# Kernel tuning notes

Measured on AMD Instinct MI355X. Metric: run time of the kernel, lower is better.

## Reference

```python
import jax, jax.numpy as jnp
import numpy as np

GAMMA = 1.0e6  # sigmoid sharpness for soft histogram


def _dct_basis():
    # Standard orthonormal 8x8 2D DCT-II basis, laid out as [64, 1, 8, 8] (OIHW).
    i = np.arange(8)
    a = np.where(i == 0, np.sqrt(1.0 / 8.0), np.sqrt(2.0 / 8.0))
    cos = np.cos((2 * i[None, :] + 1) * i[:, None] * np.pi / 16.0)  # [freq, pos]
    basis = np.einsum('u,v,ui,vj->uvij', a, a, cos, cos).reshape(64, 1, 8, 8)
    return jnp.asarray(basis, jnp.float32)


def _conv(x, w, stride=1, pad=0):
    return jax.lax.conv_general_dilated(
        x, w, (stride, stride), [(pad, pad), (pad, pad)],
        dimension_numbers=('NCHW', 'OIHW', 'NCHW'))


def _bn(x, g, b, eps=1e-5):
    # BatchNorm2d in training mode: batch statistics over (N, H, W).
    m = x.mean((0, 2, 3), keepdims=True)
    v = x.var((0, 2, 3), keepdims=True)
    return g[None, :, None, None] * (x - m) * jax.lax.rsqrt(v + eps) + b[None, :, None, None]


def _pool2(x):
    return jax.lax.reduce_window(x, -jnp.inf, jax.lax.max,
                                 (1, 1, 2, 2), (1, 1, 2, 2), 'VALID')


def setup_inputs() -> dict:
    key = jax.random.key(0)
    ks = jax.random.split(key, 16)
    B = 64

    def n(k, shape, scale=0.05):
        return jax.random.normal(k, shape, jnp.float32) * scale

    FC1_IN = 15 * 8 * 256 + 64  # 30784
    return {
        'x': jax.random.normal(ks[0], (B, 1, 256, 256), jnp.float32),
        'qvectors': jax.random.uniform(ks[1], (B, 64), dtype=jnp.float32),
        'dct_basis': _dct_basis(),
        'w1a': n(ks[2], (64, 1, 5, 5)), 'b1a': jnp.zeros(64, jnp.float32),
        'g1a': jnp.ones(64, jnp.float32), 'be1a': jnp.zeros(64, jnp.float32),
        'w1b': n(ks[3], (64, 64, 5, 5)), 'b1b': jnp.zeros(64, jnp.float32),
        'g1b': jnp.ones(64, jnp.float32), 'be1b': jnp.zeros(64, jnp.float32),
        'w2a': n(ks[4], (128, 64, 5, 5)), 'b2a': jnp.zeros(128, jnp.float32),
        'g2a': jnp.ones(128, jnp.float32), 'be2a': jnp.zeros(128, jnp.float32),
        'w3a': n(ks[5], (256, 128, 5, 5)), 'b3a': jnp.zeros(256, jnp.float32),
        'g3a': jnp.ones(256, jnp.float32), 'be3a': jnp.zeros(256, jnp.float32),
        'fc1_w': n(ks[6], (500, FC1_IN), 0.02), 'fc1_b': jnp.zeros(500, jnp.float32),
        'fc2_w': n(ks[7], (500, 564), 0.02), 'fc2_b': jnp.zeros(500, jnp.float32),
        'fc3_w': n(ks[8], (2, 564), 0.02), 'fc3_b': jnp.zeros(2, jnp.float32),
    }


def reference(x, qvectors, dct_basis,
              w1a, b1a, g1a, be1a,
              w1b, b1b, g1b, be1b,
              w2a, b2a, g2a, be2a,
              w3a, b3a, g3a, be3a,
              fc1_w, fc1_b, fc2_w, fc2_b, fc3_w, fc3_b):
    # --- no_grad block: DCT + 121-bin soft histogram ---
    xd = _conv(x, dct_basis, stride=8)  # [B, 64, 32, 32]
    bins = jnp.arange(-60, 61, dtype=xd.dtype)  # 121 thresholds

    def step(_, b):
        h = jnp.sum(jax.nn.sigmoid(GAMMA * (xd - b)), axis=(2, 3)) / 1024.0  # [B, 64]
        return None, h

    _, hist = jax.lax.scan(step, None, bins)        # [121, B, 64]
    hist = jnp.transpose(hist, (1, 0, 2))           # [B, 121, 64]
    feat = hist[:, 0:120, :] - hist[:, 1:121, :]    # per-bin soft counts
    feat = jax.lax.stop_gradient(feat.reshape(-1, 1, 120, 64))

    # --- CNN stack ---
    h = jax.nn.relu(_bn(_conv(feat, w1a, pad=2) + b1a[None, :, None, None], g1a, be1a))
    h = jax.nn.relu(_bn(_conv(h, w1b, pad=2) + b1b[None, :, None, None], g1b, be1b))
    h = _pool2(h)  # [B, 64, 60, 32]
    h = jax.nn.relu(_bn(_conv(h, w2a, pad=2) + b2a[None, :, None, None], g2a, be2a))
    h = _pool2(h)  # [B, 128, 30, 16]
    h = jax.nn.relu(_bn(_conv(h, w3a, pad=2) + b3a[None, :, None, None], g3a, be3a))
    h = _pool2(h)  # [B, 256, 15, 8]

    # --- MLP head with qvector concats ---
    hf = h.reshape(-1, 15 * 8 * 256)
    z = jax.nn.relu(jnp.concatenate([qvectors, hf], axis=1) @ fc1_w.T + fc1_b)
    z = jax.nn.relu(jnp.concatenate([qvectors, z], axis=1) @ fc2_w.T + fc2_b)
    return jnp.concatenate([qvectors, z], axis=1) @ fc3_w.T + fc3_b  # [B, 2]
```

## Files before the change

### kernel.cpp

```cpp
#include <hip/hip_runtime.h>
#include <math.h>


typedef __attribute__((ext_vector_type(8))) _Float16 f16x8;
typedef __attribute__((ext_vector_type(4))) float f32x4;

#define GAMMA_F 1.0e6f

__device__ __forceinline__ unsigned short f2h(float f) {
  _Float16 h = (_Float16)f;
  union { _Float16 h; unsigned short u; } x; x.h = h; return x.u;
}
__device__ __forceinline__ float h2f(unsigned short u) {
  union { unsigned short u; _Float16 h; } x; x.u = u; return (float)x.h;
}

__global__ __launch_bounds__(256) void k_dct(const float* __restrict__ x,
                                             const float* __restrict__ basis,
                                             float* __restrict__ xd) {
  __shared__ float bT[4096];
  __shared__ float pix[4][64];
  int tid = threadIdx.x;
  for (int e = tid; e < 4096; e += 256)
    bT[e] = basis[(e & 63) * 64 + (e >> 6)];
  __syncthreads();
  int w = tid >> 6, lane = tid & 63;
  int b = blockIdx.x >> 3;
  int br = ((blockIdx.x & 7) << 2) + w;
  const float* xb = x + (size_t)b * 65536;
  float* xdb = xd + (size_t)b * 65536;
  for (int bc = 0; bc < 32; ++bc) {
    __syncthreads();
    pix[w][lane] = xb[(br * 8 + (lane >> 3)) * 256 + bc * 8 + (lane & 7)];
    __syncthreads();
    float acc = 0.f;
#pragma unroll
    for (int p = 0; p < 64; ++p)
      acc = fmaf(bT[p * 64 + lane], pix[w][p], acc);
    xdb[lane * 1024 + br * 32 + bc] = acc;
  }
}

__global__ __launch_bounds__(256) void k_hist(const float* __restrict__ xd,
                                              float* __restrict__ feat) {
  __shared__ float h[120];
  int tid = threadIdx.x;
  int bc = blockIdx.x;
  int b = bc >> 6, c = bc & 63;
  if (tid < 120) h[tid] = 0.f;
  __syncthreads();
  const float4* p4 = (const float4*)(xd + (size_t)bc * 1024);
  float4 v4 = p4[tid];
#pragma unroll
  for (int k = 0; k < 4; ++k) {
    float pv = k == 0 ? v4.x : (k == 1 ? v4.y : (k == 2 ? v4.z : v4.w));
    float v = rintf(pv);
    float d = pv - v;
    if (fabsf(d) < 2e-5f && v >= -60.f && v <= 60.f) {
      float s = 1.f / (1.f + expf(-GAMMA_F * d));
      int vi = (int)v;
      if (vi >= -59) atomicAdd(&h[vi + 59], 1.f - s);
      if (vi <= 59)  atomicAdd(&h[vi + 60], s);
    } else {
      int j = (int)ceilf(pv + 60.f) - 1;
      if (j >= 0 && j <= 119) atomicAdd(&h[j], 1.f);
    }
  }
  __syncthreads();
  if (tid < 120)
    feat[((size_t)b * 120 + tid) * 64 + c] = h[tid] * (1.f / 1024.f);
}

__global__ __launch_bounds__(256) void k_prepw(const float* __restrict__ w,
                                               unsigned short* __restrict__ wt,
                                               int OC, int IC) {
  int n = OC * IC * 25;
  int idx = blockIdx.x * 256 + threadIdx.x;
  if (idx >= n) return;
  int j = idx & 7;
  int q = (idx >> 3) & 3;
  int l15 = (idx >> 5) & 15;
  int r = idx >> 9;
  int icb = r % (IC / 32);
  int r2 = r / (IC / 32);
  int mt = r2 % (OC / 16);
  int t = r2 / (OC / 16);
  int oc = mt * 16 + l15;
  int ic = icb * 32 + q * 8 + j;
  wt[idx] = f2h(w[((size_t)oc * IC + ic) * 25 + t]);
}

__global__ __launch_bounds__(256) void k_conv1a(const float* __restrict__ in,
                                                const float* __restrict__ wgt,
                                                unsigned short* __restrict__ out) {
  __shared__ float tile[20 * 21];
  int tx = threadIdx.x & 15, ty = threadIdx.x >> 4;
  int tileX = (blockIdx.x & 3) * 16, tileY = (blockIdx.x >> 2) * 16;
  int b = blockIdx.y, ocb = blockIdx.z * 8;
  const float* inc = in + (size_t)b * 7680;
  for (int e = threadIdx.x; e < 400; e += 256) {
    int ly = e / 20, lx = e % 20;
    int gy = tileY - 2 + ly, gx = tileX - 2 + lx;
    float v = 0.f;
    if ((unsigned)gy < 120u && (unsigned)gx < 64u) v = inc[gy * 64 + gx];
    tile[ly * 21 + lx] = v;
  }
  __syncthreads();
  float tv[25];
#pragma unroll
  for (int dy = 0; dy < 5; ++dy)
#pragma unroll
    for (int dx = 0; dx < 5; ++dx)
      tv[dy * 5 + dx] = tile[(ty + dy) * 21 + tx + dx];
  float acc[8];
#pragma unroll
  for (int o = 0; o < 8; ++o) {
    const float* wo = wgt + (size_t)(ocb + o) * 25;
    float a = 0.f;
#pragma unroll
    for (int t = 0; t < 25; ++t) a = fmaf(tv[t], wo[t], a);
    acc[o] = a;
  }
  int oy = tileY + ty, ox = tileX + tx;
  if (oy < 120) {
    size_t base = (((size_t)b * 120 + oy) * 64 + ox) * 64 + ocb;
    ushort4 p0, p1;
    p0.x = f2h(acc[0]); p0.y = f2h(acc[1]); p0.z = f2h(acc[2]); p0.w = f2h(acc[3]);
    p1.x = f2h(acc[4]); p1.y = f2h(acc[5]); p1.z = f2h(acc[6]); p1.w = f2h(acc[7]);
    *(ushort4*)(out + base) = p0;
    *(ushort4*)(out + base + 4) = p1;
  }
}

template <int CIN, int H, int W, int TC, int NT, int OC, bool PREBN>
__global__ __launch_bounds__(256, 3) void k_convM(const unsigned short* __restrict__ in,
                                                  const unsigned short* __restrict__ wt,
                                                  unsigned short* __restrict__ out,
                                                  const float* __restrict__ pst,
                                                  const float* __restrict__ pg,
                                                  const float* __restrict__ pbe) {
  constexpr int XC = TC / 16, RPW = NT / XC, WGR = 4 * RPW;
  constexpr int LW = TC + 4, LR = WGR + 4, NPX = LR * LW;
  constexpr int NXC = W / TC;
  constexpr int MTS = (CIN / 32) * 512;
  constexpr int TS = (OC / 16) * MTS;
  __shared__ unsigned short lds[NPX * 40];
  int tid = threadIdx.x;
  int w = tid >> 6, lane = tid & 63, l15 = lane & 15, q = lane >> 4;
  int q4 = tid & 3;
  int ry = blockIdx.x / NXC, cx = blockIdx.x % NXC;
  int y0 = ry * WGR, x0 = cx * TC;
  int b = blockIdx.y, oc0 = blockIdx.z * 64;
  int z4 = blockIdx.z * 4;
  int lofs = (l15 * 4 + q) * 8;
  f32x4 acc[4][NT];
#pragma unroll
  for (int mt = 0; mt < 4; ++mt)
#pragma unroll
    for (int nt = 0; nt < NT; ++nt) acc[mt][nt] = 0.f;

  for (int icb = 0; icb < CIN / 32; ++icb) {
    float s8[8], a8[8];
    if (PREBN) {
      int cb = icb * 32 + q4 * 8;
#pragma unroll
      for (int j = 0; j < 8; ++j) {
        float m = pst[cb + j], iv = pst[CIN + cb + j];
        s8[j] = pg[cb + j] * iv;
        a8[j] = pbe[cb + j] - m * s8[j];
      }
    }
    __syncthreads();
    for (int e = tid; e < NPX * 4; e += 256) {
      int px = e >> 2;
      int lr = px / LW, c = px % LW;
      int y = y0 - 2 + lr, x = x0 - 2 + c;
      f16x8 v = (f16x8)0;
      if ((unsigned)y < (unsigned)H && (unsigned)x < (unsigned)W) {
        v = *(const f16x8*)(in + (((size_t)b * H + y) * W + x) * CIN + icb * 32 + q4 * 8);
        if (PREBN) {
#pragma unroll
          for (int j = 0; j < 8; ++j) {
            float f = fmaf((float)v[j], s8[j], a8[j]);
            v[j] = (_Float16)(f > 0.f ? f : 0.f);
          }
        }
      }
      *(f16x8*)&lds[(size_t)(px * 5 + q4) * 8] = v;
    }
    __syncthreads();
    const unsigned short* wbase = wt + (size_t)icb * 512 + lofs;
    f16x8 avn[4];
#pragma unroll
    for (int mt = 0; mt < 4; ++mt)
      avn[mt] = *(const f16x8*)(wbase + (size_t)(z4 + mt) * MTS);
#pragma unroll
    for (int t = 0; t < 25; ++t) {
      int dy = t / 5, dx = t % 5;
      f16x8 avc[4];
#pragma unroll
      for (int mt = 0; mt < 4; ++mt) avc[mt] = avn[mt];
      if (t < 24) {
#pragma unroll
        for (int mt = 0; mt < 4; ++mt)
          avn[mt] = *(const f16x8*)(wbase + (size_t)(t + 1) * TS + (size_t)(z4 + mt) * MTS);
      }
#pragma unroll
      for (int nt = 0; nt < NT; ++nt) {
        int lr = w * RPW + nt / XC + dy;
        int c = (nt % XC) * 16 + l15 + dx;
        f16x8 bv = *(const f16x8*)&lds[(size_t)((lr * LW + c) * 5 + q) * 8];
#pragma unroll
        for (int mt = 0; mt < 4; ++mt)
          acc[mt][nt] = __builtin_amdgcn_mfma_f32_16x16x32_f16(avc[mt], bv, acc[mt][nt], 0, 0, 0);
      }
    }
  }
#pragma unroll
  for (int nt = 0; nt < NT; ++nt) {
    int y = y0 + w * RPW + nt / XC;
    if (y >= H) continue;
    int x = x0 + (nt % XC) * 16 + l15;
    size_t pbase = (((size_t)b * H + y) * W + x) * OC + oc0 + q * 4;
#pragma unroll
    for (int mt = 0; mt < 4; ++mt) {
      ushort4 pk;
      pk.x = f2h(acc[mt][nt][0]);
      pk.y = f2h(acc[mt][nt][1]);
      pk.z = f2h(acc[mt][nt][2]);
      pk.w = f2h(acc[mt][nt][3]);
      *(ushort4*)(out + pbase + mt * 16) = pk;
    }
  }
}

template <int C>
__global__ __launch_bounds__(256) void k_bnstatsv(const unsigned short* __restrict__ x,
                                                  float* __restrict__ acc,
                                                  int nIter) {
  constexpr int CV = C / 8, KPB = 256 / CV;
  __shared__ float r1[256][8], r2[256][8];
  int tid = threadIdx.x;
  int cv = tid % CV, kq = tid / CV;
  size_t row0 = (size_t)blockIdx.x * (KPB * nIter) + kq;
  const unsigned short* p = x + row0 * C + cv * 8;
  float s1[8], s2[8];
#pragma unroll
  for (int j = 0; j < 8; ++j) { s1[j] = 0.f; s2[j] = 0.f; }
  for (int it = 0; it < nIter; ++it) {
    f16x8 v = *(const f16x8*)(p + (size_t)it * KPB * C);
#pragma unroll
    for (int j = 0; j < 8; ++j) {
      float f = (float)v[j];
      s1[j] += f;
      s2[j] += f * f;
    }
  }
#pragma unroll
  for (int j = 0; j < 8; ++j) { r1[tid][j] = s1[j]; r2[tid][j] = s2[j]; }
  __syncthreads();
  if (tid < C) {
    int cv0 = tid >> 3, e = tid & 7;
    float t1 = 0.f, t2 = 0.f;
    for (int k = 0; k < KPB; ++k) {
      t1 += r1[k * CV + cv0][e];
      t2 += r2[k * CV + cv0][e];
    }
    atomicAdd(&acc[tid], t1);
    atomicAdd(&acc[C + tid], t2);
  }
}

__global__ __launch_bounds__(256) void k_bnfin(const float* __restrict__ acc,
                                               float* __restrict__ stats,
                                               int C, float invN) {
  int c = threadIdx.x + blockIdx.x * 256;
  if (c >= C) return;
  float m = acc[c] * invN;
  float v = acc[C + c] * invN - m * m;
  stats[c] = m;
  stats[C + c] = rsqrtf(v + 1e-5f);
}

template <int C, int H, int W>
__global__ __launch_bounds__(256) void k_brp(const unsigned short* __restrict__ x,
                                             unsigned short* __restrict__ y,
                                             const float* __restrict__ stats,
                                             const float* __restrict__ g,
                                             const float* __restrict__ be) {
  constexpr int OH = H / 2, OW = W / 2, CV = C / 8;
  int idx = blockIdx.x * 256 + threadIdx.x;
  int cv = idx % CV;
  int t = idx / CV;
  int ox = t % OW; t /= OW;
  int oy = t % OH;
  int b = t / OH;
  int c0 = cv * 8;
  const unsigned short* p = x + ((size_t)(b * H + oy * 2) * W + ox * 2) * C + c0;
  f16x8 v00 = *(const f16x8*)p;
  f16x8 v01 = *(const f16x8*)(p + C);
  f16x8 v10 = *(const f16x8*)(p + (size_t)W * C);
  f16x8 v11 = *(const f16x8*)(p + (size_t)W * C + C);
  f16x8 r;
#pragma unroll
  for (int j = 0; j < 8; ++j) {
    int c = c0 + j;
    float m = stats[c], iv = stats[C + c], gg = g[c], bb = be[c];
    float f0 = gg * (((float)v00[j] - m) * iv) + bb;
    float f1 = gg * (((float)v01[j] - m) * iv) + bb;
    float f2 = gg * (((float)v10[j] - m) * iv) + bb;
    float f3 = gg * (((float)v11[j] - m) * iv) + bb;
    f0 = f0 > 0.f ? f0 : 0.f;
    f1 = f1 > 0.f ? f1 : 0.f;
    f2 = f2 > 0.f ? f2 : 0.f;
    f3 = f3 > 0.f ? f3 : 0.f;
    float r01 = f0 > f1 ? f0 : f1;
    float r23 = f2 > f3 ? f2 : f3;
    r[j] = (_Float16)(r01 > r23 ? r01 : r23);
  }
  *(f16x8*)(y + (size_t)idx * 8) = r;
}

__global__ __launch_bounds__(256) void k_brp3t(const unsigned short* __restrict__ x,
                                               unsigned short* __restrict__ actT,
                                               const float* __restrict__ stats,
                                               const float* __restrict__ g,
                                               const float* __restrict__ be) {
  __shared__ float tile[64 * 65];
  int s = blockIdx.x;
  int oy = s >> 3, ox = s & 7;
  int ci = threadIdx.x & 63, bq = threadIdx.x >> 6;
  for (int cs = 0; cs < 4; ++cs) {
    int c = cs * 64 + ci;
    float m = stats[c], iv = stats[256 + c], gg = g[c], bb = be[c];
    __syncthreads();
    for (int b = bq; b < 64; b += 4) {
      float mx = 0.f;
#pragma unroll
      for (int qq = 0; qq < 4; ++qq) {
        int yy = oy * 2 + (qq >> 1), xx = ox * 2 + (qq & 1);
        float v = h2f(x[((size_t)(b * 30 + yy) * 16 + xx) * 256 + c]);
        v = gg * ((v - m) * iv) + bb;
        v = v > 0.f ? v : 0.f;
        mx = v > mx ? v : mx;
      }
      tile[ci * 65 + b] = mx;
    }
    __syncthreads();
    for (int e = threadIdx.x; e < 4096; e += 256) {
      int cc = e >> 6, bb2 = e & 63;
      actT[(size_t)bb2 * 30784 + 64 + (cs * 64 + cc) * 120 + s] = f2h(tile[cc * 65 + bb2]);
    }
  }
}

__global__ __launch_bounds__(256) void k_qinit(const float* __restrict__ q,
                                               unsigned short* __restrict__ actT,
                                               float* __restrict__ in2T,
                                               float* __restrict__ in3T,
                                               float* __restrict__ z1pre,
                                               float* __restrict__ bnacc) {
  int idx = blockIdx.x * 256 + threadIdx.x;
  if (idx < 32000) z1pre[idx] = 0.f;
  else if (idx < 33024) bnacc[idx - 32000] = 0.f;
  if (idx >= 4096) return;
  int b = idx >> 6, i = idx & 63;
  float v = q[idx];
  actT[(size_t)b * 30784 + i] = f2h(v);
  in2T[i * 64 + b] = v;
  in3T[i * 64 + b] = v;
}

__global__ __launch_bounds__(256) void k_fc1m(const unsigned short* __restrict__ actT,
                                              const float* __restrict__ wgt,
                                              float* __restrict__ z1pre) {
  constexpr int IN = 30784;
  constexpr int KSTEPS = IN / 32;
  __shared__ float part[4][16][64];
  int tid = threadIdx.x;
  int w = tid >> 6, lane = tid & 63, l15 = lane & 15, q = lane >> 4;
  int ob = blockIdx.x * 16;
  int row = ob + l15; if (row > 499) row = 499;
  int kw = blockIdx.y * 4 + w;
  f32x4 acc[4];
#pragma unroll
  for (int nt = 0; nt < 4; ++nt) acc[nt] = 0.f;
  for (int s = kw; s < KSTEPS; s += 32) {
    int k0 = s * 32;
    const float4* wp = (const float4*)(wgt + (size_t)row * IN + k0 + q * 8);
    float4 wa = wp[0], wb = wp[1];
    f16x8 a;
    a[0] = (_Float16)wa.x; a[1] = (_Float16)wa.y;
    a[2] = (_Float16)wa.z; a[3] = (_Float16)wa.w;
    a[4] = (_Float16)wb.x; a[5] = (_Float16)wb.y;
    a[6] = (_Float16)wb.z; a[7] = (_Float16)wb.w;
#pragma unroll
    for (int nt = 0; nt < 4; ++nt) {
      f16x8 bv = *(const f16x8*)(actT + (size_t)(nt * 16 + l15) * IN + k0 + q * 8);
      acc[nt] = __builtin_amdgcn_mfma_f32_16x16x32_f16(a, bv, acc[nt], 0, 0, 0);
    }
  }
#pragma unroll
  for (int nt = 0; nt < 4; ++nt)
#pragma unroll
    for (int reg = 0; reg < 4; ++reg)
      part[w][q * 4 + reg][nt * 16 + l15] = acc[nt][reg];
  __syncthreads();
  for (int e = tid; e < 1024; e += 256) {
    int m = e >> 6, n = e & 63;
    float sum = part[0][m][n] + part[1][m][n] + part[2][m][n] + part[3][m][n];
    int o = ob + m;
    if (o < 500) atomicAdd(&z1pre[o * 64 + n], sum);
  }
}

__global__ __launch_bounds__(256) void k_fc1ep(const float* __restrict__ z1pre,
                                               const float* __restrict__ bias,
                                               float* __restrict__ in2T) {
  int idx = blockIdx.x * 256 + threadIdx.x;
  if (idx >= 500 * 64) return;
  int o = idx >> 6;
  float v = z1pre[idx] + bias[o];
  in2T[idx + 64 * 64] = v > 0.f ? v : 0.f;
}

__global__ __launch_bounds__(256) void k_fc_small(const float* __restrict__ inT,
                                                  const float* __restrict__ wgt,
                                                  const float* __restrict__ bias,
                                                  float* __restrict__ out,
                                                  int IN, int mode) {
  __shared__ float part[4][64];
  int o = blockIdx.x;
  int lane = threadIdx.x & 63, w = threadIdx.x >> 6;
  float acc = 0.f;
  for (int i = w; i < IN; i += 4)
    acc = fmaf(inT[(size_t)i * 64 + lane], wgt[(size_t)o * IN + i], acc);
  part[w][lane] = acc;
  __syncthreads();
  if (threadIdx.x < 64) {
    float s = part[0][lane] + part[1][lane] + part[2][lane] + part[3][lane] + bias[o];
    if (mode == 0) {
      s = s > 0.f ? s : 0.f;
      out[(64 + o) * 64 + lane] = s;
    } else {
      out[lane * 2 + o] = s;
    }
  }
}

extern "C" void kernel_launch(void* const* d_in, const int* in_sizes, int n_in,
                              void* d_out, int out_size, void* d_ws, size_t ws_size,
                              hipStream_t stream) {
  const float* x      = (const float*)d_in[0];
  const float* qvec   = (const float*)d_in[1];
  const float* basis  = (const float*)d_in[2];
  const float* w1a    = (const float*)d_in[3];
  const float* g1a    = (const float*)d_in[5];
  const float* be1a   = (const float*)d_in[6];
  const float* w1b    = (const float*)d_in[7];
  const float* g1b    = (const float*)d_in[9];
  const float* be1b   = (const float*)d_in[10];
  const float* w2a    = (const float*)d_in[11];
  const float* g2a    = (const float*)d_in[13];
  const float* be2a   = (const float*)d_in[14];
  const float* w3a    = (const float*)d_in[15];
  const float* g3a    = (const float*)d_in[17];
  const float* be3a   = (const float*)d_in[18];
  const float* fc1w   = (const float*)d_in[19];
  const float* fc1b   = (const float*)d_in[20];
  const float* fc2w   = (const float*)d_in[21];
  const float* fc2b   = (const float*)d_in[22];
  const float* fc3w   = (const float*)d_in[23];
  const float* fc3b   = (const float*)d_in[24];
  float* out = (float*)d_out;

  char* base = (char*)d_ws;
  constexpr size_t ARENA = 62914560;
  char* arenaA = base;
  char* arenaB = base + ARENA;
  char* sm     = base + 2 * ARENA;

  float*          xd   = (float*)arenaA;
  unsigned short* A    = (unsigned short*)arenaA;
  unsigned short* P1   = (unsigned short*)arenaA;
  unsigned short* P2   = (unsigned short*)arenaA;
  unsigned short* actT = (unsigned short*)arenaA;

  float*          feat = (float*)arenaB;
  unsigned short* Bb   = (unsigned short*)arenaB;
  unsigned short* C2   = (unsigned short*)arenaB;
  unsigned short* D3   = (unsigned short*)arenaB;

  float* in2T = (float*)sm;
  float* in3T = (float*)(sm + 144384);
  float* z1p  = (float*)(sm + 288768);
  float* ACC  = (float*)(sm + 416768);
  float* S1A  = (float*)(sm + 420864);
  float* S1B  = (float*)(sm + 421376);
  float* S2A  = (float*)(sm + 421888);
  float* S3A  = (float*)(sm + 422912);
  unsigned short* WT1 = (unsigned short*)(sm + 424960);
  unsigned short* WT2 = (unsigned short*)(sm + 834560);
  unsigned short* WT3 = (unsigned short*)(sm + 1653760);

  k_qinit<<<130, 256, 0, stream>>>(qvec, actT, in2T, in3T, z1p, ACC);
  k_prepw<<<400, 256, 0, stream>>>(w1b, WT1, 64, 64);
  k_prepw<<<800, 256, 0, stream>>>(w2a, WT2, 128, 64);
  k_prepw<<<3200, 256, 0, stream>>>(w3a, WT3, 256, 128);

  k_dct<<<64 * 8, 256, 0, stream>>>(x, basis, xd);
  k_hist<<<4096, 256, 0, stream>>>(xd, feat);

  k_conv1a<<<dim3(32, 64, 8), 256, 0, stream>>>(feat, w1a, A);
  k_bnstatsv<64><<<240, 256, 0, stream>>>(A, ACC, 64);
  k_bnfin<<<1, 64, 0, stream>>>(ACC, S1A, 64, 1.f / 491520.f);

  k_convM<64, 120, 64, 64, 4, 64, true><<<dim3(30, 64, 1), 256, 0, stream>>>(
      A, WT1, Bb, S1A, g1a, be1a);
  k_bnstatsv<64><<<240, 256, 0, stream>>>(Bb, ACC + 128, 64);
  k_bnfin<<<1, 64, 0, stream>>>(ACC + 128, S1B, 64, 1.f / 491520.f);
  k_brp<64, 120, 64><<<3840, 256, 0, stream>>>(Bb, P1, S1B, g1b, be1b);

  k_convM<64, 60, 32, 32, 4, 128, false><<<dim3(8, 64, 2), 256, 0, stream>>>(
      P1, WT2, C2, S1A, g1a, be1a);
  k_bnstatsv<128><<<240, 256, 0, stream>>>(C2, ACC + 256, 32);
  k_bnfin<<<1, 128, 0, stream>>>(ACC + 256, S2A, 128, 1.f / 122880.f);
  k_brp<128, 60, 32><<<1920, 256, 0, stream>>>(C2, P2, S2A, g2a, be2a);

  k_convM<128, 30, 16, 16, 2, 256, false><<<dim3(4, 64, 4), 256, 0, stream>>>(
      P2, WT3, D3, S1A, g1a, be1a);
  k_bnstatsv<256><<<240, 256, 0, stream>>>(D3, ACC + 512, 16);
  k_bnfin<<<1, 256, 0, stream>>>(ACC + 512, S3A, 256, 1.f / 30720.f);
  k_qinit<<<130, 256, 0, stream>>>(qvec, actT, in2T, in3T, z1p, ACC);
  k_brp3t<<<120, 256, 0, stream>>>(D3, actT, S3A, g3a, be3a);

  k_fc1m<<<dim3(32, 8), 256, 0, stream>>>(actT, fc1w, z1p);
  k_fc1ep<<<125, 256, 0, stream>>>(z1p, fc1b, in2T);
  k_fc_small<<<500, 256, 0, stream>>>(in2T, fc2w, fc2b, in3T, 564, 0);
  k_fc_small<<<2, 256, 0, stream>>>(in3T, fc3w, fc3b, out, 564, 1);
}
```

Baseline: 889.3 us.

## Fuse BatchNorm statistics accumulation into conv epilogues, drop separate stats kernels

The conv1a and the MFMA conv kernels now reduce per-channel sum and sum-of-squares in their epilogues, using wave shuffles and shared memory, then atomically add the totals to the BN accumulator. This removes four k_bnstatsv launches that each re-read the full fp16 activation tensors. The cost is extra epilogue work and more atomics per block. Statistics are now taken from the fp32 accumulators instead of the fp16-rounded values, which changes numerics slightly.

New measurement: 941.0 us. 5.8% more time.

```diff
diff --git a/kernel.cpp b/kernel.cpp
--- a/kernel.cpp
+++ b/kernel.cpp
@@ -92,9 +92,12 @@
 
 __global__ __launch_bounds__(256) void k_conv1a(const float* __restrict__ in,
                                                 const float* __restrict__ wgt,
-                                                unsigned short* __restrict__ out) {
+                                                unsigned short* __restrict__ out,
+                                                float* __restrict__ bnacc) {
   __shared__ float tile[20 * 21];
+  __shared__ float reds[2][4][8];
   int tx = threadIdx.x & 15, ty = threadIdx.x >> 4;
+  int lane = threadIdx.x & 63, wv = threadIdx.x >> 6;
   int tileX = (blockIdx.x & 3) * 16, tileY = (blockIdx.x >> 2) * 16;
   int b = blockIdx.y, ocb = blockIdx.z * 8;
   const float* inc = in + (size_t)b * 7680;
@@ -122,7 +125,8 @@
     acc[o] = a;
   }
   int oy = tileY + ty, ox = tileX + tx;
-  if (oy < 120) {
+  bool valid = oy < 120;
+  if (valid) {
     size_t base = (((size_t)b * 120 + oy) * 64 + ox) * 64 + ocb;
     ushort4 p0, p1;
     p0.x = f2h(acc[0]); p0.y = f2h(acc[1]); p0.z = f2h(acc[2]); p0.w = f2h(acc[3]);
@@ -130,6 +134,23 @@
     *(ushort4*)(out + base) = p0;
     *(ushort4*)(out + base + 4) = p1;
   }
+#pragma unroll
+  for (int o = 0; o < 8; ++o) {
+    float v = valid ? acc[o] : 0.f;
+    float v2 = v * v;
+#pragma unroll
+    for (int m = 1; m < 64; m <<= 1) {
+      v += __shfl_xor(v, m);
+      v2 += __shfl_xor(v2, m);
+    }
+    if (lane == 0) { reds[0][wv][o] = v; reds[1][wv][o] = v2; }
+  }
+  __syncthreads();
+  if (threadIdx.x < 16) {
+    int o = threadIdx.x & 7, s = threadIdx.x >> 3;
+    float t = reds[s][0][o] + reds[s][1][o] + reds[s][2][o] + reds[s][3][o];
+    atomicAdd(&bnacc[s * 64 + ocb + o], t);
+  }
 }
 
 template <int CIN, int H, int W, int TC, int NT, int OC, bool PREBN>
@@ -138,7 +159,8 @@
                                                   unsigned short* __restrict__ out,
                                                   const float* __restrict__ pst,
                                                   const float* __restrict__ pg,
-                                                  const float* __restrict__ pbe) {
+                                                  const float* __restrict__ pbe,
+                                                  float* __restrict__ bnacc) {
   constexpr int XC = TC / 16, RPW = NT / XC, WGR = 4 * RPW;
   constexpr int LW = TC + 4, LR = WGR + 4, NPX = LR * LW;
   constexpr int NXC = W / TC;
@@ -216,6 +238,11 @@
       }
     }
   }
+  float s1[4][4], s2[4][4];
+#pragma unroll
+  for (int mt = 0; mt < 4; ++mt)
+#pragma unroll
+    for (int r = 0; r < 4; ++r) { s1[mt][r] = 0.f; s2[mt][r] = 0.f; }
 #pragma unroll
   for (int nt = 0; nt < NT; ++nt) {
     int y = y0 + w * RPW + nt / XC;
@@ -230,44 +257,45 @@
       pk.z = f2h(acc[mt][nt][2]);
       pk.w = f2h(acc[mt][nt][3]);
       *(ushort4*)(out + pbase + mt * 16) = pk;
-    }
-  }
-}
-
-template <int C>
-__global__ __launch_bounds__(256) void k_bnstatsv(const unsigned short* __restrict__ x,
-                                                  float* __restrict__ acc,
-                                                  int nIter) {
-  constexpr int CV = C / 8, KPB = 256 / CV;
-  __shared__ float r1[256][8], r2[256][8];
-  int tid = threadIdx.x;
-  int cv = tid % CV, kq = tid / CV;
-  size_t row0 = (size_t)blockIdx.x * (KPB * nIter) + kq;
-  const unsigned short* p = x + row0 * C + cv * 8;
-  float s1[8], s2[8];
-#pragma unroll
-  for (int j = 0; j < 8; ++j) { s1[j] = 0.f; s2[j] = 0.f; }
-  for (int it = 0; it < nIter; ++it) {
-    f16x8 v = *(const f16x8*)(p + (size_t)it * KPB * C);
-#pragma unroll
-    for (int j = 0; j < 8; ++j) {
-      float f = (float)v[j];
-      s1[j] += f;
-      s2[j] += f * f;
-    }
-  }
-#pragma unroll
-  for (int j = 0; j < 8; ++j) { r1[tid][j] = s1[j]; r2[tid][j] = s2[j]; }
-  __syncthreads();
-  if (tid < C) {
-    int cv0 = tid >> 3, e = tid & 7;
-    float t1 = 0.f, t2 = 0.f;
-    for (int k = 0; k < KPB; ++k) {
-      t1 += r1[k * CV + cv0][e];
-      t2 += r2[k * CV + cv0][e];
-    }
-    atomicAdd(&acc[tid], t1);
-    atomicAdd(&acc[C + tid], t2);
+#pragma unroll
+      for (int r = 0; r < 4; ++r) {
+        float v = acc[mt][nt][r];
+        s1[mt][r] += v;
+        s2[mt][r] += v * v;
+      }
+    }
+  }
+#pragma unroll
+  for (int mt = 0; mt < 4; ++mt)
+#pragma unroll
+    for (int r = 0; r < 4; ++r) {
+#pragma unroll
+      for (int m = 1; m < 16; m <<= 1) {
+        s1[mt][r] += __shfl_xor(s1[mt][r], m);
+        s2[mt][r] += __shfl_xor(s2[mt][r], m);
+      }
+    }
+  __syncthreads();
+  float* red = (float*)lds;
+  if (l15 == 0) {
+#pragma unroll
+    for (int mt = 0; mt < 4; ++mt)
+#pragma unroll
+      for (int r = 0; r < 4; ++r) {
+        int slot = ((w * 4 + q) * 16 + mt * 4 + r) * 2;
+        red[slot] = s1[mt][r];
+        red[slot + 1] = s2[mt][r];
+      }
+  }
+  __syncthreads();
+  if (tid < 128) {
+    int c = tid & 63, s = tid >> 6;
+    int mt = c >> 4, q2 = (c >> 2) & 3, r = c & 3;
+    float t = 0.f;
+#pragma unroll
+    for (int ww = 0; ww < 4; ++ww)
+      t += red[((ww * 4 + q2) * 16 + mt * 4 + r) * 2 + s];
+    atomicAdd(&bnacc[s * OC + oc0 + c], t);
   }
 }
 
@@ -511,25 +539,21 @@
   k_dct<<<64 * 8, 256, 0, stream>>>(x, basis, xd);
   k_hist<<<4096, 256, 0, stream>>>(xd, feat);
 
-  k_conv1a<<<dim3(32, 64, 8), 256, 0, stream>>>(feat, w1a, A);
-  k_bnstatsv<64><<<240, 256, 0, stream>>>(A, ACC, 64);
+  k_conv1a<<<dim3(32, 64, 8), 256, 0, stream>>>(feat, w1a, A, ACC);
   k_bnfin<<<1, 64, 0, stream>>>(ACC, S1A, 64, 1.f / 491520.f);
 
   k_convM<64, 120, 64, 64, 4, 64, true><<<dim3(30, 64, 1), 256, 0, stream>>>(
-      A, WT1, Bb, S1A, g1a, be1a);
-  k_bnstatsv<64><<<240, 256, 0, stream>>>(Bb, ACC + 128, 64);
+      A, WT1, Bb, S1A, g1a, be1a, ACC + 128);
   k_bnfin<<<1, 64, 0, stream>>>(ACC + 128, S1B, 64, 1.f / 491520.f);
   k_brp<64, 120, 64><<<3840, 256, 0, stream>>>(Bb, P1, S1B, g1b, be1b);
 
   k_convM<64, 60, 32, 32, 4, 128, false><<<dim3(8, 64, 2), 256, 0, stream>>>(
-      P1, WT2, C2, S1A, g1a, be1a);
-  k_bnstatsv<128><<<240, 256, 0, stream>>>(C2, ACC + 256, 32);
+      P1, WT2, C2, S1A, g1a, be1a, ACC + 256);
   k_bnfin<<<1, 128, 0, stream>>>(ACC + 256, S2A, 128, 1.f / 122880.f);
   k_brp<128, 60, 32><<<1920, 256, 0, stream>>>(C2, P2, S2A, g2a, be2a);
 
   k_convM<128, 30, 16, 16, 2, 256, false><<<dim3(4, 64, 4), 256, 0, stream>>>(
-      P2, WT3, D3, S1A, g1a, be1a);
-  k_bnstatsv<256><<<240, 256, 0, stream>>>(D3, ACC + 512, 16);
+      P2, WT3, D3, S1A, g1a, be1a, ACC + 512);
   k_bnfin<<<1, 256, 0, stream>>>(ACC + 512, S3A, 256, 1.f / 30720.f);
   k_qinit<<<130, 256, 0, stream>>>(qvec, actT, in2T, in3T, z1p, ACC);
   k_brp3t<<<120, 256, 0, stream>>>(D3, actT, S3A, g3a, be3a);
```

## Fuse DCT and soft histogram into one kernel with shared-memory partial histograms

Applied to the files above, without the earlier changes.

The DCT kernel now bins each coefficient directly into a per-block shared-memory histogram (64 channels x 120 bins) instead of writing the full DCT image to global memory for a separate histogram kernel. Each block then adds its partial histograms into the feature buffer with global atomics, and the init kernel is enlarged to zero that buffer first. This removes a 16 MB write and re-read plus one launch, at the cost of 30 KB extra shared memory per block (lower occupancy), shared-memory atomic contention, and 7680 global atomics per block across 8 blocks per image. Because the partial sums are added in varying order, results are no longer bit-for-bit deterministic.

Result: slower. 1.040 ms (+16.9%).

```diff
diff --git a/kernel.cpp b/kernel.cpp
--- a/kernel.cpp
+++ b/kernel.cpp
@@ -15,20 +15,21 @@
   union { unsigned short u; _Float16 h; } x; x.u = u; return (float)x.h;
 }
 
-__global__ __launch_bounds__(256) void k_dct(const float* __restrict__ x,
-                                             const float* __restrict__ basis,
-                                             float* __restrict__ xd) {
+__global__ __launch_bounds__(256) void k_dcth(const float* __restrict__ x,
+                                              const float* __restrict__ basis,
+                                              float* __restrict__ feat) {
   __shared__ float bT[4096];
   __shared__ float pix[4][64];
+  __shared__ float hist[64 * 120];
   int tid = threadIdx.x;
   for (int e = tid; e < 4096; e += 256)
     bT[e] = basis[(e & 63) * 64 + (e >> 6)];
+  for (int e = tid; e < 7680; e += 256) hist[e] = 0.f;
   __syncthreads();
   int w = tid >> 6, lane = tid & 63;
   int b = blockIdx.x >> 3;
   int br = ((blockIdx.x & 7) << 2) + w;
   const float* xb = x + (size_t)b * 65536;
-  float* xdb = xd + (size_t)b * 65536;
   for (int bc = 0; bc < 32; ++bc) {
     __syncthreads();
     pix[w][lane] = xb[(br * 8 + (lane >> 3)) * 256 + bc * 8 + (lane & 7)];
@@ -37,38 +38,23 @@
 #pragma unroll
     for (int p = 0; p < 64; ++p)
       acc = fmaf(bT[p * 64 + lane], pix[w][p], acc);
-    xdb[lane * 1024 + br * 32 + bc] = acc;
-  }
-}
-
-__global__ __launch_bounds__(256) void k_hist(const float* __restrict__ xd,
-                                              float* __restrict__ feat) {
-  __shared__ float h[120];
-  int tid = threadIdx.x;
-  int bc = blockIdx.x;
-  int b = bc >> 6, c = bc & 63;
-  if (tid < 120) h[tid] = 0.f;
-  __syncthreads();
-  const float4* p4 = (const float4*)(xd + (size_t)bc * 1024);
-  float4 v4 = p4[tid];
-#pragma unroll
-  for (int k = 0; k < 4; ++k) {
-    float pv = k == 0 ? v4.x : (k == 1 ? v4.y : (k == 2 ? v4.z : v4.w));
-    float v = rintf(pv);
-    float d = pv - v;
+    float v = rintf(acc);
+    float d = acc - v;
     if (fabsf(d) < 2e-5f && v >= -60.f && v <= 60.f) {
       float s = 1.f / (1.f + expf(-GAMMA_F * d));
       int vi = (int)v;
-      if (vi >= -59) atomicAdd(&h[vi + 59], 1.f - s);
-      if (vi <= 59)  atomicAdd(&h[vi + 60], s);
+      if (vi >= -59) atomicAdd(&hist[lane * 120 + vi + 59], 1.f - s);
+      if (vi <= 59)  atomicAdd(&hist[lane * 120 + vi + 60], s);
     } else {
-      int j = (int)ceilf(pv + 60.f) - 1;
-      if (j >= 0 && j <= 119) atomicAdd(&h[j], 1.f);
+      int j = (int)ceilf(acc + 60.f) - 1;
+      if (j >= 0 && j <= 119) atomicAdd(&hist[lane * 120 + j], 1.f);
     }
   }
   __syncthreads();
-  if (tid < 120)
-    feat[((size_t)b * 120 + tid) * 64 + c] = h[tid] * (1.f / 1024.f);
+  for (int e = tid; e < 7680; e += 256) {
+    int c = e / 120, j = e % 120;
+    atomicAdd(&feat[((size_t)b * 120 + j) * 64 + c], hist[e] * (1.f / 1024.f));
+  }
 }
 
 __global__ __launch_bounds__(256) void k_prepw(const float* __restrict__ w,
@@ -359,8 +345,10 @@
                                                float* __restrict__ in2T,
                                                float* __restrict__ in3T,
                                                float* __restrict__ z1pre,
-                                               float* __restrict__ bnacc) {
+                                               float* __restrict__ bnacc,
+                                               float* __restrict__ featz) {
   int idx = blockIdx.x * 256 + threadIdx.x;
+  if (featz && idx < 491520) featz[idx] = 0.f;
   if (idx < 32000) z1pre[idx] = 0.f;
   else if (idx < 33024) bnacc[idx - 32000] = 0.f;
   if (idx >= 4096) return;
@@ -480,7 +468,6 @@
   char* arenaB = base + ARENA;
   char* sm     = base + 2 * ARENA;
 
-  float*          xd   = (float*)arenaA;
   unsigned short* A    = (unsigned short*)arenaA;
   unsigned short* P1   = (unsigned short*)arenaA;
   unsigned short* P2   = (unsigned short*)arenaA;
@@ -503,13 +490,12 @@
   unsigned short* WT2 = (unsigned short*)(sm + 834560);
   unsigned short* WT3 = (unsigned short*)(sm + 1653760);
 
-  k_qinit<<<130, 256, 0, stream>>>(qvec, actT, in2T, in3T, z1p, ACC);
+  k_qinit<<<1920, 256, 0, stream>>>(qvec, actT, in2T, in3T, z1p, ACC, feat);
   k_prepw<<<400, 256, 0, stream>>>(w1b, WT1, 64, 64);
   k_prepw<<<800, 256, 0, stream>>>(w2a, WT2, 128, 64);
   k_prepw<<<3200, 256, 0, stream>>>(w3a, WT3, 256, 128);
 
-  k_dct<<<64 * 8, 256, 0, stream>>>(x, basis, xd);
-  k_hist<<<4096, 256, 0, stream>>>(xd, feat);
+  k_dcth<<<64 * 8, 256, 0, stream>>>(x, basis, feat);
 
   k_conv1a<<<dim3(32, 64, 8), 256, 0, stream>>>(feat, w1a, A);
   k_bnstatsv<64><<<240, 256, 0, stream>>>(A, ACC, 64);
@@ -531,7 +517,7 @@
       P2, WT3, D3, S1A, g1a, be1a);
   k_bnstatsv<256><<<240, 256, 0, stream>>>(D3, ACC + 512, 16);
   k_bnfin<<<1, 256, 0, stream>>>(ACC + 512, S3A, 256, 1.f / 30720.f);
-  k_qinit<<<130, 256, 0, stream>>>(qvec, actT, in2T, in3T, z1p, ACC);
+  k_qinit<<<130, 256, 0, stream>>>(qvec, actT, in2T, in3T, z1p, ACC, nullptr);
   k_brp3t<<<120, 256, 0, stream>>>(D3, actT, S3A, g3a, be3a);
 
   k_fc1m<<<dim3(32, 8), 256, 0, stream>>>(actT, fc1w, z1p);
```
